# Kernel tuning notes

Measured on AMD Instinct MI355X. Metric: run time of the kernel, lower is better.

Reference implementation:

```python
import jax, jax.numpy as jnp
import numpy as np

N = 100000       # nodes
E = 1600000      # edges
EA = 7           # edge_attr_dim
H = 64           # hidden_dim
L = 32           # latent_dim
G = 512          # graphs in batch
C = 6            # num_classes


def _gin_conv(x, src, dst, edge_attr, We, be, W1, b1, W2, b2, eps):
    # GINE-style: message = relu(x_j + edge_proj), sum-aggregate at dst, then 2-layer MLP
    m = jax.nn.relu(x[src] + edge_attr @ We + be)            # [E, d_in]
    agg = jax.ops.segment_sum(m, dst, num_segments=x.shape[0])
    h = (1.0 + eps) * x + agg                                # [N, d_in]
    return jax.nn.relu(h @ W1 + b1) @ W2 + b2                # [N, H]


def setup_inputs() -> dict:
    key = jax.random.key(0)
    ks = jax.random.split(key, 24)
    s = 0.05
    inp = {
        "x": jax.random.normal(ks[0], (N,), jnp.float32),
        "edge_index": jax.random.randint(ks[1], (2, E), 0, N, jnp.int64),
        "edge_attr": jax.random.uniform(ks[2], (E, EA), jnp.float32),
        "batch": jnp.sort(jax.random.randint(ks[3], (N,), 0, G, jnp.int64)),
        # conv1 (input dim 1)
        "We1": jax.random.normal(ks[4], (EA, 1), jnp.float32) * s,
        "be1": jnp.zeros((1,), jnp.float32),
        "W11": jax.random.normal(ks[5], (1, H), jnp.float32) * s,
        "b11": jnp.zeros((H,), jnp.float32),
        "W12": jax.random.normal(ks[6], (H, H), jnp.float32) * s,
        "b12": jnp.zeros((H,), jnp.float32),
        "eps1": jnp.float32(0.0),
        # conv2 (input dim H)
        "We2": jax.random.normal(ks[7], (EA, H), jnp.float32) * s,
        "be2": jnp.zeros((H,), jnp.float32),
        "W21": jax.random.normal(ks[8], (H, H), jnp.float32) * s,
        "b21": jnp.zeros((H,), jnp.float32),
        "W22": jax.random.normal(ks[9], (H, H), jnp.float32) * s,
        "b22": jnp.zeros((H,), jnp.float32),
        "eps2": jnp.float32(0.0),
        # heads
        "Wmu": jax.random.normal(ks[10], (H, L), jnp.float32) * s,
        "bmu": jnp.zeros((L,), jnp.float32),
        "Wlv": jax.random.normal(ks[11], (H, L), jnp.float32) * s,
        "blv": jnp.zeros((L,), jnp.float32),
        "Wc": jax.random.normal(ks[12], (L, C), jnp.float32) * s,
        "bc": jnp.zeros((C,), jnp.float32),
    }
    return inp


def reference(x, edge_index, edge_attr, batch,
              We1, be1, W11, b11, W12, b12, eps1,
              We2, be2, W21, b21, W22, b22, eps2,
              Wmu, bmu, Wlv, blv, Wc, bc):
    src, dst = edge_index[0], edge_index[1]
    h = x.reshape(-1, 1)                                        # [N,1]
    h = jax.nn.relu(_gin_conv(h, src, dst, edge_attr, We1, be1, W11, b11, W12, b12, eps1))
    h = jax.nn.relu(_gin_conv(h, src, dst, edge_attr, We2, be2, W21, b21, W22, b22, eps2))
    mu = h @ Wmu + bmu                                          # [N,L]
    logvar = h @ Wlv + blv                                      # [N,L]
    # reparameterize (training path)
    noise = jax.random.normal(jax.random.key(42), mu.shape, mu.dtype)
    z = mu + noise * jnp.exp(0.5 * logvar)
    # global mean pool over graphs
    zsum = jax.ops.segment_sum(z, batch, num_segments=G)        # [G,L]
    cnt = jax.ops.segment_sum(jnp.ones((z.shape[0],), z.dtype), batch, num_segments=G)
    graph_emb = zsum / jnp.maximum(cnt, 1.0)[:, None]
    class_logits = graph_emb @ Wc + bc                          # [G,C]
    return (z, mu, logvar, class_logits)
```

## Files before the change

### kernel.cpp

```cpp
#include <hip/hip_runtime.h>
#include <stdint.h>

#define N_NODES 100000
#define N_EDGES 1600000
#define EAD 7
#define H 64
#define LAT 32
#define NG 512
#define NC 6
#define NZ (N_NODES * LAT)

#define NB_SCAN 391
#define NPW1 4
#define NPWM 8

static_assert(N_NODES % (4 * NPW1) == 0, "conv1 grid exact");
static_assert(N_NODES % (4 * NPWM) == 0, "conv2_heads grid exact");
static_assert(N_EDGES % 256 == 0, "edge grid exact");

__device__ __forceinline__ void threefry2x32_42(uint32_t& x0, uint32_t& x1) {
    const uint32_t k0 = 0u, k1 = 42u;
    const uint32_t k2 = k0 ^ k1 ^ 0x1BD11BDAu;
    x0 += k0; x1 += k1;
#define TF_ROUND(r) { x0 += x1; x1 = (x1 << (r)) | (x1 >> (32 - (r))); x1 ^= x0; }
    TF_ROUND(13) TF_ROUND(15) TF_ROUND(26) TF_ROUND(6)
    x0 += k1; x1 += k2 + 1u;
    TF_ROUND(17) TF_ROUND(29) TF_ROUND(16) TF_ROUND(24)
    x0 += k2; x1 += k0 + 2u;
    TF_ROUND(13) TF_ROUND(15) TF_ROUND(26) TF_ROUND(6)
    x0 += k0; x1 += k1 + 3u;
    TF_ROUND(17) TF_ROUND(29) TF_ROUND(16) TF_ROUND(24)
    x0 += k1; x1 += k2 + 4u;
    TF_ROUND(13) TF_ROUND(15) TF_ROUND(26) TF_ROUND(6)
    x0 += k2; x1 += k0 + 5u;
#undef TF_ROUND
}

__device__ __forceinline__ float erfinv_f32(float x) {
    float w = -log1pf(-x * x);
    float p;
    if (w < 5.0f) {
        w = w - 2.5f;
        p = 2.81022636e-08f;
        p = fmaf(p, w, 3.43273939e-07f);
        p = fmaf(p, w, -3.5233877e-06f);
        p = fmaf(p, w, -4.39150654e-06f);
        p = fmaf(p, w, 0.00021858087f);
        p = fmaf(p, w, -0.00125372503f);
        p = fmaf(p, w, -0.00417768164f);
        p = fmaf(p, w, 0.246640727f);
        p = fmaf(p, w, 1.50140941f);
    } else {
        w = sqrtf(w) - 3.0f;
        p = -0.000200214257f;
        p = fmaf(p, w, 0.000100950558f);
        p = fmaf(p, w, 0.00134934322f);
        p = fmaf(p, w, -0.00367342844f);
        p = fmaf(p, w, 0.00573950773f);
        p = fmaf(p, w, -0.0076224613f);
        p = fmaf(p, w, 0.00943887047f);
        p = fmaf(p, w, 1.00167406f);
        p = fmaf(p, w, 2.83297682f);
    }
    return p * x;
}

__global__ void hist_k(const int* __restrict__ dst, int* __restrict__ deg) {
    int e = blockIdx.x * blockDim.x + threadIdx.x;
    if (e < N_EDGES) atomicAdd(&deg[dst[e]], 1);
}

__global__ void scan1_k(const int* __restrict__ deg, int* __restrict__ bsum) {
    __shared__ int sv[256];
    int t = threadIdx.x, i = blockIdx.x * 256 + t;
    sv[t] = (i < N_NODES) ? deg[i] : 0;
    __syncthreads();
    for (int o = 128; o > 0; o >>= 1) {
        if (t < o) sv[t] += sv[t + o];
        __syncthreads();
    }
    if (t == 0) bsum[blockIdx.x] = sv[0];
}

__global__ void scan2_k(int* __restrict__ bsum) {
    __shared__ int sv[512];
    int t = threadIdx.x;
    int v = (t < NB_SCAN) ? bsum[t] : 0;
    sv[t] = v;
    __syncthreads();
    for (int o = 1; o < 512; o <<= 1) {
        int a = (t >= o) ? sv[t - o] : 0;
        __syncthreads();
        sv[t] += a;
        __syncthreads();
    }
    if (t < NB_SCAN) bsum[t] = sv[t] - v;
}

__global__ void scan3_k(const int* __restrict__ deg, const int* __restrict__ bsum,
                        int* __restrict__ off, int* __restrict__ cur) {
    __shared__ int sv[256];
    int t = threadIdx.x, i = blockIdx.x * 256 + t;
    int v = (i < N_NODES) ? deg[i] : 0;
    sv[t] = v;
    __syncthreads();
    for (int o = 1; o < 256; o <<= 1) {
        int a = (t >= o) ? sv[t - o] : 0;
        __syncthreads();
        sv[t] += a;
        __syncthreads();
    }
    if (i < N_NODES) {
        int s = bsum[blockIdx.x] + sv[t] - v;
        off[i] = s;
        cur[i] = s;
    }
}

__global__ void scatter_k(const float* __restrict__ x, const int* __restrict__ src,
                          const int* __restrict__ dst, const float* __restrict__ ea,
                          const float* __restrict__ We1, const float* __restrict__ be1,
                          int* __restrict__ cur, int2* __restrict__ rec8,
                          float* __restrict__ m1s) {
    int e = blockIdx.x * blockDim.x + threadIdx.x;
    if (e >= N_EDGES) return;
    int s = src[e], d = dst[e];
    const float* ep = ea + (size_t)e * EAD;
    float p = be1[0];
#pragma unroll
    for (int k = 0; k < EAD; k++) p = fmaf(ep[k], We1[k], p);
    float m = x[s] + p;
    m = m > 0.0f ? m : 0.0f;
    int pos = atomicAdd(&cur[d], 1);
    rec8[pos] = make_int2(s, e);
    m1s[pos] = m;
}

__global__ void conv1_fused(const float* __restrict__ x, const float* __restrict__ m1s,
                            const int* __restrict__ off, const int* __restrict__ cur,
                            const float* __restrict__ W11, const float* __restrict__ b11,
                            const float* __restrict__ W12, const float* __restrict__ b12,
                            const float* __restrict__ eps1, float* __restrict__ hA) {
    __shared__ float sW12[H * H];
    __shared__ float stg[4][H];
    int tid = threadIdx.x;
    for (int i = tid; i < H * H; i += 256) sW12[i] = W12[i];
    int w = tid >> 6, lane = tid & 63;
    float rW11 = W11[lane], rb11 = b11[lane], rb12 = b12[lane], er = eps1[0];
    __syncthreads();
    int n0 = (blockIdx.x * 4 + w) * NPW1;
#pragma unroll
    for (int ni = 0; ni < NPW1; ni++) {
        int n = n0 + ni;
        int g0 = off[n], g1 = cur[n];
        float agg = 0.0f;
        for (int j = g0 + lane; j < g1; j += 64) agg += m1s[j];
#pragma unroll
        for (int o = 32; o > 0; o >>= 1) agg += __shfl_xor(agg, o, 64);
        float xv = x[n];
        float h1 = fmaf(er, xv, xv) + agg;
        float t = fmaf(h1, rW11, rb11);
        t = t > 0.0f ? t : 0.0f;
        stg[w][lane] = t;
        float acc = rb12;
#pragma unroll
        for (int j = 0; j < H; j++) acc = fmaf(stg[w][j], sW12[j * H + lane], acc);
        hA[(size_t)n * H + lane] = acc > 0.0f ? acc : 0.0f;
    }
}

__global__ void conv2_heads(const float* __restrict__ hA, const int2* __restrict__ rec8,
                            const float* __restrict__ ea, const int* __restrict__ batch,
                            const int* __restrict__ off, const int* __restrict__ cur,
                            const float* __restrict__ We2, const float* __restrict__ be2,
                            const float* __restrict__ W21, const float* __restrict__ b21,
                            const float* __restrict__ W22, const float* __restrict__ b22,
                            const float* __restrict__ eps2,
                            const float* __restrict__ Wmu, const float* __restrict__ bmu,
                            const float* __restrict__ Wlv, const float* __restrict__ blv,
                            float4* __restrict__ out4, float* __restrict__ zsum) {
    __shared__ float sW21[H * H], sW22[H * H];
    __shared__ float sWm[H * LAT], sWl[H * LAT];
    __shared__ float4 srec[4][64][2];
    __shared__ float stg[4][H];
    __shared__ float4 szout[4][3][NPWM][LAT / 4];
    int tid = threadIdx.x;
    for (int i = tid; i < H * H; i += 256) { sW21[i] = W21[i]; sW22[i] = W22[i]; }
    for (int i = tid; i < H * LAT; i += 256) { sWm[i] = Wmu[i]; sWl[i] = Wlv[i]; }
    int w = tid >> 6, lane = tid & 63;
    float rW[EAD];
#pragma unroll
    for (int k = 0; k < EAD; k++) rW[k] = We2[k * H + lane];
    float rbe2 = be2[lane], rb21 = b21[lane], rb22 = b22[lane], er = eps2[0];
    int l = lane & 31;
    float rbh = (lane < LAT) ? bmu[l] : blv[l];
    __syncthreads();

    int n0 = (blockIdx.x * 4 + w) * NPWM;
    int eend = cur[n0 + NPWM - 1];
    int sbase = -(1 << 30);

    auto restage = [&](int g) {
        sbase = g;
        int cnt = eend - g; cnt = cnt > 64 ? 64 : cnt;
        float a0 = 0, a1 = 0, a2 = 0, a3 = 0, a4 = 0, a5 = 0, a6 = 0;
        int s = 0;
        if (lane < cnt) {
            int2 r = rec8[g + lane];
            s = r.x;
            const float* ep = ea + (size_t)r.y * EAD;
            a0 = ep[0]; a1 = ep[1]; a2 = ep[2]; a3 = ep[3];
            a4 = ep[4]; a5 = ep[5]; a6 = ep[6];
        }
        srec[w][lane][0] = make_float4(a0, a1, a2, a3);
        srec[w][lane][1] = make_float4(a4, a5, a6, __int_as_float(s));
    };

    for (int ni = 0; ni < NPWM; ni++) {
        int n = n0 + ni;
        int g = off[n], gend = cur[n];
        float acc = 0.0f;
        while (g + 4 <= gend) {
            if (g + 4 > sbase + 64) restage(g);
            int b = g - sbase;
            float4 A0 = srec[w][b + 0][0], B0 = srec[w][b + 0][1];
            float4 A1 = srec[w][b + 1][0], B1 = srec[w][b + 1][1];
            float4 A2 = srec[w][b + 2][0], B2 = srec[w][b + 2][1];
            float4 A3 = srec[w][b + 3][0], B3 = srec[w][b + 3][1];
            int s0 = __builtin_amdgcn_readfirstlane(__float_as_int(B0.w));
            int s1 = __builtin_amdgcn_readfirstlane(__float_as_int(B1.w));
            int s2 = __builtin_amdgcn_readfirstlane(__float_as_int(B2.w));
            int s3 = __builtin_amdgcn_readfirstlane(__float_as_int(B3.w));
            float hv0 = hA[(size_t)s0 * H + lane];
            float hv1 = hA[(size_t)s1 * H + lane];
            float hv2 = hA[(size_t)s2 * H + lane];
            float hv3 = hA[(size_t)s3 * H + lane];
            float p0 = rbe2, p1 = rbe2, p2 = rbe2, p3 = rbe2;
            p0 = fmaf(A0.x, rW[0], p0); p0 = fmaf(A0.y, rW[1], p0);
            p0 = fmaf(A0.z, rW[2], p0); p0 = fmaf(A0.w, rW[3], p0);
            p0 = fmaf(B0.x, rW[4], p0); p0 = fmaf(B0.y, rW[5], p0);
            p0 = fmaf(B0.z, rW[6], p0);
            p1 = fmaf(A1.x, rW[0], p1); p1 = fmaf(A1.y, rW[1], p1);
            p1 = fmaf(A1.z, rW[2], p1); p1 = fmaf(A1.w, rW[3], p1);
            p1 = fmaf(B1.x, rW[4], p1); p1 = fmaf(B1.y, rW[5], p1);
            p1 = fmaf(B1.z, rW[6], p1);
            p2 = fmaf(A2.x, rW[0], p2); p2 = fmaf(A2.y, rW[1], p2);
            p2 = fmaf(A2.z, rW[2], p2); p2 = fmaf(A2.w, rW[3], p2);
            p2 = fmaf(B2.x, rW[4], p2); p2 = fmaf(B2.y, rW[5], p2);
            p2 = fmaf(B2.z, rW[6], p2);
            p3 = fmaf(A3.x, rW[0], p3); p3 = fmaf(A3.y, rW[1], p3);
            p3 = fmaf(A3.z, rW[2], p3); p3 = fmaf(A3.w, rW[3], p3);
            p3 = fmaf(B3.x, rW[4], p3); p3 = fmaf(B3.y, rW[5], p3);
            p3 = fmaf(B3.z, rW[6], p3);
            acc += fmaxf(hv0 + p0, 0.0f);
            acc += fmaxf(hv1 + p1, 0.0f);
            acc += fmaxf(hv2 + p2, 0.0f);
            acc += fmaxf(hv3 + p3, 0.0f);
            g += 4;
        }
        while (g < gend) {
            if (g >= sbase + 64) restage(g);
            int b = g - sbase;
            float4 A = srec[w][b][0], B = srec[w][b][1];
            int s = __builtin_amdgcn_readfirstlane(__float_as_int(B.w));
            float hv = hA[(size_t)s * H + lane];
            float p = rbe2;
            p = fmaf(A.x, rW[0], p); p = fmaf(A.y, rW[1], p);
            p = fmaf(A.z, rW[2], p); p = fmaf(A.w, rW[3], p);
            p = fmaf(B.x, rW[4], p); p = fmaf(B.y, rW[5], p);
            p = fmaf(B.z, rW[6], p);
            acc += fmaxf(hv + p, 0.0f);
            g++;
        }
        float hself = hA[(size_t)n * H + lane];
        float h2 = fmaf(er, hself, hself) + acc;
        stg[w][lane] = h2;
        float t = rb21;
#pragma unroll
        for (int j = 0; j < H; j++) t = fmaf(stg[w][j], sW21[j * H + lane], t);
        t = t > 0.0f ? t : 0.0f;
        stg[w][lane] = t;
        float o2 = rb22;
#pragma unroll
        for (int j = 0; j < H; j++) o2 = fmaf(stg[w][j], sW22[j * H + lane], o2);
        o2 = o2 > 0.0f ? o2 : 0.0f;
        stg[w][lane] = o2;
        const float* Wh = (lane < LAT) ? sWm : sWl;
        float v = rbh;
#pragma unroll
        for (int j = 0; j < H; j++) v = fmaf(stg[w][j], Wh[j * LAT + l], v);
        float o = __shfl(v, lane ^ 32);
        if (lane < LAT) {
            float muv = v, lvv = o;
            int i = n * LAT + l;
            uint32_t x0 = 0u, x1 = (uint32_t)i;
            threefry2x32_42(x0, x1);
            uint32_t bits = x0 ^ x1;
            float f = __uint_as_float((bits >> 9) | 0x3F800000u) - 1.0f;
            const float lo = -0.99999994f;
            float u = fmaxf(lo, fmaf(f, 2.0f, lo));
            float noise = 1.41421356237309515f * erfinv_f32(u);
            float z = fmaf(noise, expf(0.5f * lvv), muv);
            float* zp = (float*)&szout[w][0][ni][0];
            float* mp = (float*)&szout[w][1][ni][0];
            float* lp = (float*)&szout[w][2][ni][0];
            zp[l] = z; mp[l] = muv; lp[l] = lvv;
            int bg = batch[n];
            atomicAdd(&zsum[bg * LAT + l], z);
        }
    }
    int nl = lane >> 3, f4 = lane & 7;
#pragma unroll
    for (int it = 0; it < 3; it++)
        out4[(size_t)it * (NZ / 4) + (size_t)(n0 + nl) * 8 + f4] = szout[w][it][nl][f4];
}

__global__ void pool2_k(const float* __restrict__ zsum, const int* __restrict__ batch,
                        const float* __restrict__ Wc, const float* __restrict__ bc,
                        float* __restrict__ out) {
    __shared__ float emb[LAT];
    int g = blockIdx.x, tid = threadIdx.x;
    int lo = 0, hi = N_NODES;
    while (lo < hi) { int mid = (lo + hi) >> 1; if (batch[mid] < g) lo = mid + 1; else hi = mid; }
    int start = lo;
    hi = N_NODES;
    while (lo < hi) { int mid = (lo + hi) >> 1; if (batch[mid] < g + 1) lo = mid + 1; else hi = mid; }
    int end = lo;
    if (tid < LAT) {
        float invc = 1.0f / fmaxf((float)(end - start), 1.0f);
        emb[tid] = zsum[g * LAT + tid] * invc;
    }
    __syncthreads();
    if (tid < NC) {
        float r = bc[tid];
#pragma unroll
        for (int l = 0; l < LAT; l++) r = fmaf(emb[l], Wc[l * NC + tid], r);
        out[g * NC + tid] = r;
    }
}

extern "C" void kernel_launch(void* const* d_in, const int* in_sizes, int n_in,
                              void* d_out, int out_size, void* d_ws, size_t ws_size,
                              hipStream_t stream) {
    const float* x     = (const float*)d_in[0];
    const int*   ei    = (const int*)d_in[1];
    const float* ea    = (const float*)d_in[2];
    const int*   batch = (const int*)d_in[3];
    const float* We1   = (const float*)d_in[4];
    const float* be1   = (const float*)d_in[5];
    const float* W11   = (const float*)d_in[6];
    const float* b11   = (const float*)d_in[7];
    const float* W12   = (const float*)d_in[8];
    const float* b12   = (const float*)d_in[9];
    const float* eps1  = (const float*)d_in[10];
    const float* We2   = (const float*)d_in[11];
    const float* be2   = (const float*)d_in[12];
    const float* W21   = (const float*)d_in[13];
    const float* b21   = (const float*)d_in[14];
    const float* W22   = (const float*)d_in[15];
    const float* b22   = (const float*)d_in[16];
    const float* eps2  = (const float*)d_in[17];
    const float* Wmu   = (const float*)d_in[18];
    const float* bmu   = (const float*)d_in[19];
    const float* Wlv   = (const float*)d_in[20];
    const float* blv   = (const float*)d_in[21];
    const float* Wc    = (const float*)d_in[22];
    const float* bc    = (const float*)d_in[23];

    float* zsum = (float*)d_ws;
    int*   deg  = (int*)d_ws + NG * LAT;
    int*   off  = deg + N_NODES;
    int*   cur  = off + N_NODES;
    int*   bsum = cur + N_NODES;
    int2*  rec8 = (int2*)(bsum + 512);
    float* m1s  = (float*)(rec8 + N_EDGES);
    float* hA   = m1s + N_EDGES;
    float* outf = (float*)d_out;

    hipMemsetAsync(d_ws, 0, (size_t)(NG * LAT + N_NODES) * sizeof(float), stream);

    const int* src = ei;
    const int* dst = ei + N_EDGES;

    hist_k<<<N_EDGES / 256, 256, 0, stream>>>(dst, deg);
    scan1_k<<<NB_SCAN, 256, 0, stream>>>(deg, bsum);
    scan2_k<<<1, 512, 0, stream>>>(bsum);
    scan3_k<<<NB_SCAN, 256, 0, stream>>>(deg, bsum, off, cur);
    scatter_k<<<N_EDGES / 256, 256, 0, stream>>>(x, src, dst, ea, We1, be1, cur, rec8, m1s);
    conv1_fused<<<N_NODES / (4 * NPW1), 256, 0, stream>>>(
        x, m1s, off, cur, W11, b11, W12, b12, eps1, hA);
    conv2_heads<<<N_NODES / (4 * NPWM), 256, 0, stream>>>(
        hA, rec8, ea, batch, off, cur, We2, be2, W21, b21, W22, b22, eps2,
        Wmu, bmu, Wlv, blv, (float4*)outf, zsum);
    pool2_k<<<NG, 64, 0, stream>>>(zsum, batch, Wc, bc, outf + 3 * (size_t)NZ);
}
```

Measured before the change: 787.2 us.

## Restructure conv2_heads for 512-thread blocks with fewer nodes per wave

conv2_heads now runs 8 waves per block of 512 threads, and each wave handles 5 nodes instead of 8. The head weights Wmu/Wlv are read from global memory (cache) rather than staged in LDS, and the output staging buffer in LDS is removed. Outputs are written directly from each node iteration via lane shuffles into float4 stores. This reduces LDS use per block to raise occupancy and cut grid tail effects, but it adds global weight loads, redundant RNG work in all 64 lanes, and smaller per-node stores.

```diff
diff --git a/kernel.cpp b/kernel.cpp
--- a/kernel.cpp
+++ b/kernel.cpp
@@ -12,10 +12,10 @@
 
 #define NB_SCAN 391
 #define NPW1 4
-#define NPWM 8
+#define NPWM 5
 
 static_assert(N_NODES % (4 * NPW1) == 0, "conv1 grid exact");
-static_assert(N_NODES % (4 * NPWM) == 0, "conv2_heads grid exact");
+static_assert(N_NODES % (8 * NPWM) == 0, "conv2_heads grid exact");
 static_assert(N_EDGES % 256 == 0, "edge grid exact");
 
 __device__ __forceinline__ void threefry2x32_42(uint32_t& x0, uint32_t& x1) {
@@ -180,13 +180,10 @@
                             const float* __restrict__ Wlv, const float* __restrict__ blv,
                             float4* __restrict__ out4, float* __restrict__ zsum) {
     __shared__ float sW21[H * H], sW22[H * H];
-    __shared__ float sWm[H * LAT], sWl[H * LAT];
-    __shared__ float4 srec[4][64][2];
-    __shared__ float stg[4][H];
-    __shared__ float4 szout[4][3][NPWM][LAT / 4];
+    __shared__ float4 srec[8][64][2];
+    __shared__ float stg[8][H];
     int tid = threadIdx.x;
-    for (int i = tid; i < H * H; i += 256) { sW21[i] = W21[i]; sW22[i] = W22[i]; }
-    for (int i = tid; i < H * LAT; i += 256) { sWm[i] = Wmu[i]; sWl[i] = Wlv[i]; }
+    for (int i = tid; i < H * H; i += 512) { sW21[i] = W21[i]; sW22[i] = W22[i]; }
     int w = tid >> 6, lane = tid & 63;
     float rW[EAD];
 #pragma unroll
@@ -194,9 +191,10 @@
     float rbe2 = be2[lane], rb21 = b21[lane], rb22 = b22[lane], er = eps2[0];
     int l = lane & 31;
     float rbh = (lane < LAT) ? bmu[l] : blv[l];
-    __syncthreads();
-
-    int n0 = (blockIdx.x * 4 + w) * NPWM;
+    const float* __restrict__ Wh = (lane < LAT) ? Wmu : Wlv;
+    __syncthreads();
+
+    int n0 = (blockIdx.x * 8 + w) * NPWM;
     int eend = cur[n0 + NPWM - 1];
     int sbase = -(1 << 30);
 
@@ -285,34 +283,36 @@
         for (int j = 0; j < H; j++) o2 = fmaf(stg[w][j], sW22[j * H + lane], o2);
         o2 = o2 > 0.0f ? o2 : 0.0f;
         stg[w][lane] = o2;
-        const float* Wh = (lane < LAT) ? sWm : sWl;
         float v = rbh;
-#pragma unroll
+#pragma unroll 16
         for (int j = 0; j < H; j++) v = fmaf(stg[w][j], Wh[j * LAT + l], v);
         float o = __shfl(v, lane ^ 32);
-        if (lane < LAT) {
-            float muv = v, lvv = o;
-            int i = n * LAT + l;
-            uint32_t x0 = 0u, x1 = (uint32_t)i;
-            threefry2x32_42(x0, x1);
-            uint32_t bits = x0 ^ x1;
-            float f = __uint_as_float((bits >> 9) | 0x3F800000u) - 1.0f;
-            const float lo = -0.99999994f;
-            float u = fmaxf(lo, fmaf(f, 2.0f, lo));
-            float noise = 1.41421356237309515f * erfinv_f32(u);
-            float z = fmaf(noise, expf(0.5f * lvv), muv);
-            float* zp = (float*)&szout[w][0][ni][0];
-            float* mp = (float*)&szout[w][1][ni][0];
-            float* lp = (float*)&szout[w][2][ni][0];
-            zp[l] = z; mp[l] = muv; lp[l] = lvv;
-            int bg = batch[n];
-            atomicAdd(&zsum[bg * LAT + l], z);
+        float muv = (lane < LAT) ? v : o;
+        float lvv = (lane < LAT) ? o : v;
+        int i = n * LAT + l;
+        uint32_t x0 = 0u, x1 = (uint32_t)i;
+        threefry2x32_42(x0, x1);
+        uint32_t bits = x0 ^ x1;
+        float f = __uint_as_float((bits >> 9) | 0x3F800000u) - 1.0f;
+        const float lo = -0.99999994f;
+        float u = fmaxf(lo, fmaf(f, 2.0f, lo));
+        float noise = 1.41421356237309515f * erfinv_f32(u);
+        float z = fmaf(noise, expf(0.5f * lvv), muv);
+        if (lane < LAT) atomicAdd(&zsum[batch[n] * LAT + l], z);
+        int sl = (lane << 2) & 63;
+        float4 zv = make_float4(__shfl(z, sl), __shfl(z, sl + 1),
+                                __shfl(z, sl + 2), __shfl(z, sl + 3));
+        float4 mv = make_float4(__shfl(muv, sl), __shfl(muv, sl + 1),
+                                __shfl(muv, sl + 2), __shfl(muv, sl + 3));
+        float4 lv4 = make_float4(__shfl(lvv, sl), __shfl(lvv, sl + 1),
+                                 __shfl(lvv, sl + 2), __shfl(lvv, sl + 3));
+        if (lane < 8) {
+            size_t o8 = (size_t)n * 8 + lane;
+            out4[o8] = zv;
+            out4[(size_t)(NZ / 4) + o8] = mv;
+            out4[2 * (size_t)(NZ / 4) + o8] = lv4;
         }
     }
-    int nl = lane >> 3, f4 = lane & 7;
-#pragma unroll
-    for (int it = 0; it < 3; it++)
-        out4[(size_t)it * (NZ / 4) + (size_t)(n0 + nl) * 8 + f4] = szout[w][it][nl][f4];
 }
 
 __global__ void pool2_k(const float* __restrict__ zsum, const int* __restrict__ batch,
@@ -389,7 +389,7 @@
     scatter_k<<<N_EDGES / 256, 256, 0, stream>>>(x, src, dst, ea, We1, be1, cur, rec8, m1s);
     conv1_fused<<<N_NODES / (4 * NPW1), 256, 0, stream>>>(
         x, m1s, off, cur, W11, b11, W12, b12, eps1, hA);
-    conv2_heads<<<N_NODES / (4 * NPWM), 256, 0, stream>>>(
+    conv2_heads<<<N_NODES / (8 * NPWM), 512, 0, stream>>>(
         hA, rec8, ea, batch, off, cur, We2, be2, W21, b21, W22, b22, eps2,
         Wmu, bmu, Wlv, blv, (float4*)outf, zsum);
     pool2_k<<<NG, 64, 0, stream>>>(zsum, batch, Wc, bc, outf + 3 * (size_t)NZ);
```

New measurement: 1.115 ms. 1.42x slower.

## Aggregate conv1 messages with float atomics during degree histogram pass

Applied to the files above, without the earlier changes.

The conv1 message computation moves into the histogram kernel, which atomically adds each edge's scalar message directly into a per-node aggregate alongside the degree count. The CSR scatter no longer writes per-edge conv1 messages, and the conv1 node MLP reads the aggregate directly instead of walking CSR segments. This removes the m1s buffer writes and reads and the segmented reduction, at the cost of an extra float atomic per edge. It also makes the conv1 sum order nondeterministic.

```diff
diff --git a/kernel.cpp b/kernel.cpp
--- a/kernel.cpp
+++ b/kernel.cpp
@@ -11,10 +11,10 @@
 #define NZ (N_NODES * LAT)
 
 #define NB_SCAN 391
-#define NPW1 4
+#define C1_NPB 32
 #define NPWM 8
 
-static_assert(N_NODES % (4 * NPW1) == 0, "conv1 grid exact");
+static_assert(N_NODES % C1_NPB == 0, "conv1_node grid exact");
 static_assert(N_NODES % (4 * NPWM) == 0, "conv2_heads grid exact");
 static_assert(N_EDGES % 256 == 0, "edge grid exact");
 
@@ -65,9 +65,47 @@
     return p * x;
 }
 
-__global__ void hist_k(const int* __restrict__ dst, int* __restrict__ deg) {
+__global__ void conv1_edge(const float* __restrict__ x, const int* __restrict__ src,
+                           const int* __restrict__ dst, const float* __restrict__ ea,
+                           const float* __restrict__ We1, const float* __restrict__ be1,
+                           float* __restrict__ agg1, int* __restrict__ deg) {
     int e = blockIdx.x * blockDim.x + threadIdx.x;
-    if (e < N_EDGES) atomicAdd(&deg[dst[e]], 1);
+    if (e >= N_EDGES) return;
+    int s = src[e], d = dst[e];
+    const float* ep = ea + (size_t)e * EAD;
+    float p = be1[0];
+#pragma unroll
+    for (int k = 0; k < EAD; k++) p = fmaf(ep[k], We1[k], p);
+    float m = x[s] + p;
+    m = m > 0.0f ? m : 0.0f;
+    atomicAdd(&agg1[d], m);
+    atomicAdd(&deg[d], 1);
+}
+
+__global__ void conv1_node(const float* __restrict__ x, const float* __restrict__ agg1,
+                           const float* __restrict__ W11, const float* __restrict__ b11,
+                           const float* __restrict__ W12, const float* __restrict__ b12,
+                           const float* __restrict__ eps1, float* __restrict__ hA) {
+    __shared__ float sW12[H * H];
+    __shared__ float stg[4][H];
+    int tid = threadIdx.x;
+    for (int i = tid; i < H * H; i += 256) sW12[i] = W12[i];
+    int w = tid >> 6, lane = tid & 63;
+    float rW11 = W11[lane], rb11 = b11[lane], rb12 = b12[lane], er = eps1[0];
+    __syncthreads();
+#pragma unroll
+    for (int it = 0; it < C1_NPB / 4; it++) {
+        int n = blockIdx.x * C1_NPB + it * 4 + w;
+        float xv = x[n];
+        float h1 = fmaf(er, xv, xv) + agg1[n];
+        float t = fmaf(h1, rW11, rb11);
+        t = t > 0.0f ? t : 0.0f;
+        stg[w][lane] = t;
+        float acc = rb12;
+#pragma unroll
+        for (int j = 0; j < H; j++) acc = fmaf(stg[w][j], sW12[j * H + lane], acc);
+        hA[(size_t)n * H + lane] = acc > 0.0f ? acc : 0.0f;
+    }
 }
 
 __global__ void scan1_k(const int* __restrict__ deg, int* __restrict__ bsum) {
@@ -117,56 +155,13 @@
     }
 }
 
-__global__ void scatter_k(const float* __restrict__ x, const int* __restrict__ src,
-                          const int* __restrict__ dst, const float* __restrict__ ea,
-                          const float* __restrict__ We1, const float* __restrict__ be1,
-                          int* __restrict__ cur, int2* __restrict__ rec8,
-                          float* __restrict__ m1s) {
+__global__ void scatter_lite(const int* __restrict__ src, const int* __restrict__ dst,
+                             int* __restrict__ cur, int2* __restrict__ rec8) {
     int e = blockIdx.x * blockDim.x + threadIdx.x;
     if (e >= N_EDGES) return;
     int s = src[e], d = dst[e];
-    const float* ep = ea + (size_t)e * EAD;
-    float p = be1[0];
-#pragma unroll
-    for (int k = 0; k < EAD; k++) p = fmaf(ep[k], We1[k], p);
-    float m = x[s] + p;
-    m = m > 0.0f ? m : 0.0f;
     int pos = atomicAdd(&cur[d], 1);
     rec8[pos] = make_int2(s, e);
-    m1s[pos] = m;
-}
-
-__global__ void conv1_fused(const float* __restrict__ x, const float* __restrict__ m1s,
-                            const int* __restrict__ off, const int* __restrict__ cur,
-                            const float* __restrict__ W11, const float* __restrict__ b11,
-                            const float* __restrict__ W12, const float* __restrict__ b12,
-                            const float* __restrict__ eps1, float* __restrict__ hA) {
-    __shared__ float sW12[H * H];
-    __shared__ float stg[4][H];
-    int tid = threadIdx.x;
-    for (int i = tid; i < H * H; i += 256) sW12[i] = W12[i];
-    int w = tid >> 6, lane = tid & 63;
-    float rW11 = W11[lane], rb11 = b11[lane], rb12 = b12[lane], er = eps1[0];
-    __syncthreads();
-    int n0 = (blockIdx.x * 4 + w) * NPW1;
-#pragma unroll
-    for (int ni = 0; ni < NPW1; ni++) {
-        int n = n0 + ni;
-        int g0 = off[n], g1 = cur[n];
-        float agg = 0.0f;
-        for (int j = g0 + lane; j < g1; j += 64) agg += m1s[j];
-#pragma unroll
-        for (int o = 32; o > 0; o >>= 1) agg += __shfl_xor(agg, o, 64);
-        float xv = x[n];
-        float h1 = fmaf(er, xv, xv) + agg;
-        float t = fmaf(h1, rW11, rb11);
-        t = t > 0.0f ? t : 0.0f;
-        stg[w][lane] = t;
-        float acc = rb12;
-#pragma unroll
-        for (int j = 0; j < H; j++) acc = fmaf(stg[w][j], sW12[j * H + lane], acc);
-        hA[(size_t)n * H + lane] = acc > 0.0f ? acc : 0.0f;
-    }
 }
 
 __global__ void conv2_heads(const float* __restrict__ hA, const int2* __restrict__ rec8,
@@ -305,8 +300,7 @@
             float* mp = (float*)&szout[w][1][ni][0];
             float* lp = (float*)&szout[w][2][ni][0];
             zp[l] = z; mp[l] = muv; lp[l] = lvv;
-            int bg = batch[n];
-            atomicAdd(&zsum[bg * LAT + l], z);
+            atomicAdd(&zsum[batch[n] * LAT + l], z);
         }
     }
     int nl = lane >> 3, f4 = lane & 7;
@@ -368,27 +362,27 @@
     const float* bc    = (const float*)d_in[23];
 
     float* zsum = (float*)d_ws;
-    int*   deg  = (int*)d_ws + NG * LAT;
+    float* agg1 = zsum + NG * LAT;
+    int*   deg  = (int*)(agg1 + N_NODES);
     int*   off  = deg + N_NODES;
     int*   cur  = off + N_NODES;
     int*   bsum = cur + N_NODES;
     int2*  rec8 = (int2*)(bsum + 512);
-    float* m1s  = (float*)(rec8 + N_EDGES);
-    float* hA   = m1s + N_EDGES;
+    float* hA   = (float*)(rec8 + N_EDGES);
     float* outf = (float*)d_out;
 
-    hipMemsetAsync(d_ws, 0, (size_t)(NG * LAT + N_NODES) * sizeof(float), stream);
+    hipMemsetAsync(d_ws, 0, (size_t)(NG * LAT + 2 * N_NODES) * sizeof(float), stream);
 
     const int* src = ei;
     const int* dst = ei + N_EDGES;
 
-    hist_k<<<N_EDGES / 256, 256, 0, stream>>>(dst, deg);
+    conv1_edge<<<N_EDGES / 256, 256, 0, stream>>>(x, src, dst, ea, We1, be1, agg1, deg);
+    conv1_node<<<N_NODES / C1_NPB, 256, 0, stream>>>(
+        x, agg1, W11, b11, W12, b12, eps1, hA);
     scan1_k<<<NB_SCAN, 256, 0, stream>>>(deg, bsum);
     scan2_k<<<1, 512, 0, stream>>>(bsum);
     scan3_k<<<NB_SCAN, 256, 0, stream>>>(deg, bsum, off, cur);
-    scatter_k<<<N_EDGES / 256, 256, 0, stream>>>(x, src, dst, ea, We1, be1, cur, rec8, m1s);
-    conv1_fused<<<N_NODES / (4 * NPW1), 256, 0, stream>>>(
-        x, m1s, off, cur, W11, b11, W12, b12, eps1, hA);
+    scatter_lite<<<N_EDGES / 256, 256, 0, stream>>>(src, dst, cur, rec8);
     conv2_heads<<<N_NODES / (4 * NPWM), 256, 0, stream>>>(
         hA, rec8, ea, batch, off, cur, We2, be2, W21, b21, W22, b22, eps2,
         Wmu, bmu, Wlv, blv, (float4*)outf, zsum);
```

After: 877.7 us. +11.5%, slower.
